# Kernel optimization log

Measured on AMD Instinct MI355X. Metric: run time of the kernel, lower is better.

The kernel has to match this reference:

```python
import jax, jax.numpy as jnp
import numpy as np


def setup_inputs() -> dict:
    key = jax.random.key(0)
    k1, k2, k3, k4, k5 = jax.random.split(key, 5)
    B, ENS, XDIM, YDIM = 8, 256, 8192, 256
    return {
        "Ens_ten": jax.random.normal(k1, (B, ENS, XDIM), dtype=jnp.float32),
        "H": jax.random.normal(k2, (XDIM, YDIM), dtype=jnp.float32),
        "y_true_mean": jax.random.normal(k3, (1, YDIM), dtype=jnp.float32),
        "y_true_std": jax.random.normal(k4, (1, YDIM), dtype=jnp.float32),
        "noise": jax.random.normal(k5, (B, YDIM, ENS), dtype=jnp.float32),
    }


def reference(Ens_ten, H, y_true_mean, y_true_std, noise):
    # Ens_ten: [b, ens, xdim]; H: [xdim, ydim]
    b, ens, xdim = Ens_ten.shape
    Y = jnp.einsum('bex,xy->bey', Ens_ten, H)          # observation_func (linear)
    x_m = jnp.mean(Ens_ten, axis=1, keepdims=True)     # [b,1,xdim]
    y_m = jnp.mean(Y, axis=1, keepdims=True)           # [b,1,ydim]
    Xc = jnp.swapaxes(Ens_ten - x_m, 1, 2)             # [b,xdim,ens]
    Yc = jnp.swapaxes(Y - y_m, 1, 2)                   # [b,ydim,ens]
    C_xy = jnp.einsum('bxe,bye->bxy', Xc, Yc) / ens    # [b,xdim,ydim]
    C_yy = jnp.einsum('bue,bve->buv', Yc, Yc) / ens    # [b,ydim,ydim]
    R = jnp.diag(jnp.square(y_true_std)[0])            # [ydim,ydim], broadcasts over batch
    A = R + C_yy                                       # [b,ydim,ydim]
    # torch.linalg.solve(A, C_xy, left=False): K = C_xy @ inv(A)
    K = jnp.swapaxes(
        jnp.linalg.solve(jnp.swapaxes(A, 1, 2), jnp.swapaxes(C_xy, 1, 2)), 1, 2
    )                                                  # [b,xdim,ydim]
    R_2 = noise * jnp.square(y_true_std)[:, :, None]   # [b,ydim,ens]
    innov = y_true_mean[:, :, None] - Yc + R_2         # [b,ydim,ens]
    update = jnp.einsum('bxy,bye->bxe', K, innov)      # [b,xdim,ens]
    return Ens_ten + jnp.swapaxes(update, 1, 2)
```

## Files before the change

### kernel.cpp

```cpp
#include <hip/hip_runtime.h>

#define ENSN 256
#define XDIM 8192
#define YD 256
#define BATCH 8

#define OFF_Y   0
#define OFF_YC  524288
#define OFF_AUG 1048576
#define OFF_W   2097152
#define OFF_XM  2621440

typedef __attribute__((ext_vector_type(4))) short short4v;
typedef __attribute__((ext_vector_type(8))) short short8v;
typedef __attribute__((ext_vector_type(4))) float float4v;

__device__ __forceinline__ unsigned short f2bf_rne(float x) {
    unsigned u = __float_as_uint(x);
    u += 0x7FFFu + ((u >> 16) & 1u);
    return (unsigned short)(u >> 16);
}

__global__ __launch_bounds__(256) void k1_colmean(const float* __restrict__ E,
                                                  float* __restrict__ xm) {
    int x = blockIdx.x * 256 + threadIdx.x;
    int b = blockIdx.y;
    const float* p = E + (size_t)b * ENSN * XDIM + x;
    float s = 0.f;
    #pragma unroll 8
    for (int e = 0; e < ENSN; e++) s += p[(size_t)e * XDIM];
    xm[b * XDIM + x] = s * (1.0f / ENSN);
}

__global__ __launch_bounds__(256) void kc_h(const float* __restrict__ H,
                                            short* __restrict__ Hthi,
                                            short* __restrict__ Htlo) {
    __shared__ float T[64][65];
    int k0 = blockIdx.x * 64, n0 = blockIdx.y * 64;
    int tid = threadIdx.x;
    int c = tid & 63, g = tid >> 6;
    #pragma unroll
    for (int p = 0; p < 16; p++)
        T[g + p * 4][c] = H[(size_t)(k0 + g + p * 4) * YD + n0 + c];
    __syncthreads();
    #pragma unroll
    for (int p = 0; p < 16; p++) {
        int nn = g + p * 4;
        float v = T[c][nn];
        unsigned short h = f2bf_rne(v);
        float hf = __uint_as_float(((unsigned)h) << 16);
        unsigned short l2 = f2bf_rne(v - hf);
        Hthi[(size_t)(n0 + nn) * XDIM + k0 + c] = (short)h;
        Htlo[(size_t)(n0 + nn) * XDIM + k0 + c] = (short)l2;
    }
}

#define EST 40
#define BST 40

__global__ __launch_bounds__(512, 2) void k2m_ygemm(const float* __restrict__ E,
                                                    const short* __restrict__ Hthi,
                                                    const short* __restrict__ Htlo,
                                                    float* __restrict__ Y) {
    __shared__ __align__(16) short Ehi[64 * EST];
    __shared__ __align__(16) short Elo[64 * EST];
    __shared__ __align__(16) short Bhi[256 * BST];
    __shared__ __align__(16) short Blo[256 * BST];
    int tid = threadIdx.x;
    int lane = tid & 63;
    int w = tid >> 6;
    int m0 = blockIdx.x * 64;
    int kb0 = blockIdx.y * 512;
    int wr = (w & 1) * 32;
    int wc = (w >> 1) * 64;
    float4v acc[8];
    #pragma unroll
    for (int i = 0; i < 8; i++) acc[i] = (float4v){0.f, 0.f, 0.f, 0.f};

    int erow = tid >> 3, ecol = (tid & 7) * 4;
    int brow = tid >> 1, bhalf = (tid & 1) * 16;
    int fr = lane & 15, fg = lane >> 4;

    for (int s = 0; s < 16; s++) {
        int kb = kb0 + s * 32;
        float4 ev = *(const float4*)&E[(size_t)(m0 + erow) * XDIM + kb + ecol];
        float vv[4] = {ev.x, ev.y, ev.z, ev.w};
        short4v hi4, lo4;
        #pragma unroll
        for (int j = 0; j < 4; j++) {
            unsigned short h = f2bf_rne(vv[j]);
            float hf = __uint_as_float(((unsigned)h) << 16);
            unsigned short l2 = f2bf_rne(vv[j] - hf);
            hi4[j] = (short)h; lo4[j] = (short)l2;
        }
        *(short4v*)&Ehi[erow * EST + ecol] = hi4;
        *(short4v*)&Elo[erow * EST + ecol] = lo4;
        short8v bh0 = *(const short8v*)&Hthi[(size_t)brow * XDIM + kb + bhalf];
        short8v bh1 = *(const short8v*)&Hthi[(size_t)brow * XDIM + kb + bhalf + 8];
        short8v bl0 = *(const short8v*)&Htlo[(size_t)brow * XDIM + kb + bhalf];
        short8v bl1 = *(const short8v*)&Htlo[(size_t)brow * XDIM + kb + bhalf + 8];
        *(short8v*)&Bhi[brow * BST + bhalf]     = bh0;
        *(short8v*)&Bhi[brow * BST + bhalf + 8] = bh1;
        *(short8v*)&Blo[brow * BST + bhalf]     = bl0;
        *(short8v*)&Blo[brow * BST + bhalf + 8] = bl1;
        __syncthreads();
        short8v ah[2], al[2], bhf[4], blf[4];
        #pragma unroll
        for (int ti = 0; ti < 2; ti++) {
            ah[ti] = *(const short8v*)&Ehi[(wr + ti * 16 + fr) * EST + fg * 8];
            al[ti] = *(const short8v*)&Elo[(wr + ti * 16 + fr) * EST + fg * 8];
        }
        #pragma unroll
        for (int tj = 0; tj < 4; tj++) {
            bhf[tj] = *(const short8v*)&Bhi[(wc + tj * 16 + fr) * BST + fg * 8];
            blf[tj] = *(const short8v*)&Blo[(wc + tj * 16 + fr) * BST + fg * 8];
        }
        #pragma unroll
        for (int ti = 0; ti < 2; ti++)
            #pragma unroll
            for (int tj = 0; tj < 4; tj++) {
                int a = ti * 4 + tj;
                acc[a] = __builtin_amdgcn_mfma_f32_16x16x32_bf16(ah[ti], bhf[tj], acc[a], 0, 0, 0);
                acc[a] = __builtin_amdgcn_mfma_f32_16x16x32_bf16(ah[ti], blf[tj], acc[a], 0, 0, 0);
                acc[a] = __builtin_amdgcn_mfma_f32_16x16x32_bf16(al[ti], bhf[tj], acc[a], 0, 0, 0);
            }
        __syncthreads();
    }
    #pragma unroll
    for (int ti = 0; ti < 2; ti++)
        #pragma unroll
        for (int tj = 0; tj < 4; tj++)
            #pragma unroll
            for (int q = 0; q < 4; q++) {
                int row = m0 + wr + ti * 16 + fg * 4 + q;
                int col = wc + tj * 16 + fr;
                atomicAdd(&Y[row * YD + col], acc[ti * 4 + tj][q]);
            }
}

__global__ __launch_bounds__(256) void k3_center(const float* __restrict__ Y,
                                                 const float* __restrict__ ytm,
                                                 const float* __restrict__ ystd,
                                                 const float* __restrict__ noise,
                                                 float* __restrict__ Yc,
                                                 float* __restrict__ aug) {
    int b = blockIdx.y, tid = threadIdx.x;
    int y0 = blockIdx.x * 64;
    __shared__ float red[4][64];
    __shared__ float ym[64], tms[64], s2[64];
    __shared__ float T[64][65];
    int yl = tid & 63, q = tid >> 6;
    float s = 0.f;
    for (int e = q * 64; e < q * 64 + 64; e++)
        s += Y[(size_t)(b * ENSN + e) * YD + y0 + yl];
    red[q][yl] = s;
    __syncthreads();
    if (tid < 64) {
        ym[tid] = (red[0][tid] + red[1][tid] + red[2][tid] + red[3][tid]) * (1.0f / ENSN);
        float sd = ystd[y0 + tid];
        s2[tid] = sd * sd;
        tms[tid] = ytm[y0 + tid];
    }
    __syncthreads();
    for (int e0 = 0; e0 < ENSN; e0 += 64) {
        #pragma unroll
        for (int p = 0; p < 16; p++) {
            int er = q + p * 4;
            T[er][yl] = Y[(size_t)(b * ENSN + e0 + er) * YD + y0 + yl];
        }
        __syncthreads();
        int ec = yl;
        #pragma unroll
        for (int p = 0; p < 16; p++) {
            int yr = q + p * 4;
            int y = y0 + yr, e = e0 + ec;
            float yv = T[ec][yr] - ym[yr];
            Yc[(size_t)b * YD * ENSN + (size_t)y * ENSN + e] = yv;
            aug[(size_t)b * YD * 512 + (size_t)y * 512 + 256 + e] =
                tms[yr] - yv + noise[(size_t)b * YD * ENSN + (size_t)y * ENSN + e] * s2[yr];
        }
        __syncthreads();
    }
}

__global__ __launch_bounds__(256) void k4_cyy(const float* __restrict__ Yc,
                                              const float* __restrict__ ystd,
                                              float* __restrict__ aug) {
    __shared__ float As[16][68];
    __shared__ float Bs[16][68];
    int tid = threadIdx.x;
    int m0 = blockIdx.x * 64, n0 = blockIdx.y * 64, b = blockIdx.z;
    const float* Ycb = Yc + (size_t)b * YD * ENSN;
    int tr = tid >> 4, tc = tid & 15;
    float acc[4][4];
    #pragma unroll
    for (int i = 0; i < 4; i++)
        #pragma unroll
        for (int j = 0; j < 4; j++) acc[i][j] = 0.f;
    int al = tid & 15, am0 = tid >> 4;
    for (int k0 = 0; k0 < ENSN; k0 += 16) {
        #pragma unroll
        for (int p = 0; p < 4; p++) {
            int am = am0 + p * 16;
            As[al][am] = Ycb[(m0 + am) * ENSN + k0 + al];
            Bs[al][am] = Ycb[(n0 + am) * ENSN + k0 + al];
        }
        __syncthreads();
        #pragma unroll
        for (int kk = 0; kk < 16; kk++) {
            float4 a = *(const float4*)&As[kk][tr * 4];
            float4 bb = *(const float4*)&Bs[kk][tc * 4];
            float af[4] = {a.x, a.y, a.z, a.w};
            float bf[4] = {bb.x, bb.y, bb.z, bb.w};
            #pragma unroll
            for (int i = 0; i < 4; i++)
                #pragma unroll
                for (int j = 0; j < 4; j++) acc[i][j] += af[i] * bf[j];
        }
        __syncthreads();
    }
    float* augb = aug + (size_t)b * YD * 512;
    #pragma unroll
    for (int i = 0; i < 4; i++) {
        int u = m0 + tr * 4 + i;
        #pragma unroll
        for (int j = 0; j < 4; j++) {
            int v = n0 + tc * 4 + j;
            float val = acc[i][j] * (1.0f / ENSN);
            if (u == v) { float sv = ystd[u]; val += sv * sv; }
            augb[u * 512 + v] = val;
        }
    }
}

#define RSTP 484
#define LSTP 233

__global__ __launch_bounds__(1024, 4) void k5p_panel(float* __restrict__ aug, int c0) {
    __shared__ __align__(16) float R[32 * RSTP];
    __shared__ float Ls[32 * LSTP];
    __shared__ __align__(16) float Dg[32 * 33];
    __shared__ float invd[32];
    int b = blockIdx.x, tid = threadIdx.x;
    float* A = aug + (size_t)b * 256 * 512;
    int r5 = tid >> 5, c5 = tid & 31;
    int WR = 480 - c0;
    int W2 = 224 - c0;

    Dg[r5 * 33 + c5] = A[(c0 + r5) * 512 + c0 + c5];
    __syncthreads();
    if (tid < 32) {
        float u[32];
        #pragma unroll
        for (int c = 0; c < 32; c++) u[c] = Dg[tid * 33 + c];
        for (int j = 0; j < 31; j++) {
            float pv = __shfl(u[j], j);
            float f = u[j] / pv;
            #pragma unroll
            for (int c = 0; c < 32; c++) {
                if (c > j) {
                    float ujc = __shfl(u[c], j);
                    if (tid > j) u[c] -= f * ujc;
                }
            }
            if (tid > j) u[j] = f;
        }
        #pragma unroll
        for (int c = 0; c < 32; c++) Dg[tid * 33 + c] = u[c];
        invd[tid] = 1.0f / u[tid];
    }
    for (int cc = c5; cc < WR; cc += 32)
        R[r5 * RSTP + cc] = A[(c0 + r5) * 512 + c0 + 32 + cc];
    for (int row = r5; row < W2; row += 32)
        Ls[c5 * LSTP + row] = A[(c0 + 32 + row) * 512 + c0 + c5];
    __syncthreads();
    A[(c0 + r5) * 512 + c0 + c5] = Dg[r5 * 33 + c5];
    if (tid < WR) {
        float y[32];
        #pragma unroll
        for (int j = 0; j < 32; j++) {
            float s = R[j * RSTP + tid];
            #pragma unroll
            for (int m = 0; m < 32; m++)
                if (m < j) s -= Dg[j * 33 + m] * y[m];
            y[j] = s;
        }
        #pragma unroll
        for (int j = 0; j < 32; j++)
            A[(c0 + j) * 512 + c0 + 32 + tid] = y[j];
    }
    if (tid >= 512 && tid < 512 + W2) {
        int row = tid - 512;
        float l[32];
        #pragma unroll
        for (int j = 0; j < 32; j++) {
            float s = Ls[j * LSTP + row];
            #pragma unroll
            for (int m = 0; m < 32; m++)
                if (m < j) s -= l[m] * Dg[m * 33 + j];
            l[j] = s * invd[j];
        }
        #pragma unroll
        for (int j = 0; j < 32; j++)
            Ls[j * LSTP + row] = l[j];
    }
    __syncthreads();
    for (int row = r5; row < W2; row += 32)
        A[(c0 + 32 + row) * 512 + c0 + c5] = Ls[c5 * LSTP + row];
}

__global__ __launch_bounds__(256) void k5t_trail(float* __restrict__ aug, int c0) {
    __shared__ __align__(16) float Lt[32][36];
    __shared__ __align__(16) float Ut[32][36];
    int b = blockIdx.z, tid = threadIdx.x;
    float* A = aug + (size_t)b * 256 * 512;
    int r0  = c0 + 32 + blockIdx.x * 32;
    int cc0 = c0 + 32 + blockIdx.y * 32;
    int lr = tid >> 3, lc = (tid & 7) * 4;
    *(float4*)&Lt[lr][lc] = *(const float4*)&A[(size_t)(r0 + lr) * 512 + c0 + lc];
    *(float4*)&Ut[lr][lc] = *(const float4*)&A[(size_t)(c0 + lr) * 512 + cc0 + lc];
    __syncthreads();
    float* gp = &A[(size_t)(r0 + lr) * 512 + cc0 + lc];
    float4 acc = *(const float4*)gp;
    #pragma unroll
    for (int k = 0; k < 32; k++) {
        float lv = Lt[lr][k];
        float4 uv = *(const float4*)&Ut[k][lc];
        acc.x -= lv * uv.x;
        acc.y -= lv * uv.y;
        acc.z -= lv * uv.z;
        acc.w -= lv * uv.w;
    }
    *(float4*)gp = acc;
}

#define ZST  68
#define LBST 36

__global__ __launch_bounds__(512, 2) void k5s_solve(float* __restrict__ aug) {
    __shared__ __align__(16) float Zs[256 * ZST];
    __shared__ __align__(16) float Lb[224 * LBST];
    __shared__ __align__(16) float Dg[32 * 33];
    __shared__ float invd[32];
    int b = blockIdx.y, tid = threadIdx.x;
    float* A = aug + (size_t)b * 256 * 512;
    int cb = blockIdx.x * 64;
    int c = tid & 63, g = tid >> 6;
    int rr = tid >> 5, cc = tid & 31;

    for (int r = g; r < 256; r += 8)
        Zs[r * ZST + c] = A[r * 512 + 256 + cb + c];

    for (int p = 7; p >= 0; p--) {
        int c0 = 32 * p, na = c0;
        for (int r = rr; r < 32; r += 16)
            Dg[r * 33 + cc] = A[(c0 + r) * 512 + c0 + cc];
        for (int r = rr; r < na; r += 16)
            Lb[r * LBST + cc] = A[r * 512 + c0 + cc];
        if (tid < 32)
            invd[tid] = 1.0f / A[(c0 + tid) * 512 + c0 + tid];
        __syncthreads();
        if (tid < 64) {
            float x[32];
            #pragma unroll
            for (int j = 31; j >= 0; j--) {
                float s = Zs[(c0 + j) * ZST + tid];
                #pragma unroll
                for (int m = 0; m < 32; m++)
                    if (m > j) s -= Dg[j * 33 + m] * x[m];
                x[j] = s * invd[j];
            }
            #pragma unroll
            for (int j = 0; j < 32; j++) Zs[(c0 + j) * ZST + tid] = x[j];
        }
        __syncthreads();
        if (na > 0) {
            float z[32];
            #pragma unroll
            for (int k = 0; k < 32; k++) z[k] = Zs[(c0 + k) * ZST + c];
            for (int r = g; r < na; r += 8) {
                const float* lp = &Lb[r * LBST];
                float a0 = 0.f, a1 = 0.f, a2 = 0.f, a3 = 0.f;
                #pragma unroll
                for (int k = 0; k < 32; k += 4) {
                    float4 lv = *(const float4*)(lp + k);
                    a0 += lv.x * z[k + 0];
                    a1 += lv.y * z[k + 1];
                    a2 += lv.z * z[k + 2];
                    a3 += lv.w * z[k + 3];
                }
                Zs[r * ZST + c] -= (a0 + a1) + (a2 + a3);
            }
        }
        __syncthreads();
    }

    for (int r = g; r < 256; r += 8)
        A[r * 512 + 256 + cb + c] = Zs[r * ZST + c];
}

__global__ __launch_bounds__(256) void k6_w(const float* __restrict__ Yc,
                                            const float* __restrict__ aug,
                                            float* __restrict__ W) {
    __shared__ float As[16][68];
    __shared__ float Bs[16][68];
    int tid = threadIdx.x;
    int m0 = blockIdx.x * 64, n0 = blockIdx.y * 64, b = blockIdx.z;
    const float* Ycb = Yc + (size_t)b * YD * ENSN;
    const float* augb = aug + (size_t)b * YD * 512;
    int tr = tid >> 4, tc = tid & 15;
    float acc[4][4];
    #pragma unroll
    for (int i = 0; i < 4; i++)
        #pragma unroll
        for (int j = 0; j < 4; j++) acc[i][j] = 0.f;
    int c = tid & 63, kr0 = tid >> 6;
    for (int k0 = 0; k0 < YD; k0 += 16) {
        #pragma unroll
        for (int p = 0; p < 4; p++) {
            int kk = kr0 + p * 4;
            As[kk][c] = Ycb[(k0 + kk) * ENSN + m0 + c];
            Bs[kk][c] = augb[(k0 + kk) * 512 + 256 + n0 + c];
        }
        __syncthreads();
        #pragma unroll
        for (int kk = 0; kk < 16; kk++) {
            float4 a = *(const float4*)&As[kk][tr * 4];
            float4 bb = *(const float4*)&Bs[kk][tc * 4];
            float af[4] = {a.x, a.y, a.z, a.w};
            float bf[4] = {bb.x, bb.y, bb.z, bb.w};
            #pragma unroll
            for (int i = 0; i < 4; i++)
                #pragma unroll
                for (int j = 0; j < 4; j++) acc[i][j] += af[i] * bf[j];
        }
        __syncthreads();
    }
    float* Wb = W + (size_t)b * ENSN * ENSN;
    #pragma unroll
    for (int i = 0; i < 4; i++)
        #pragma unroll
        for (int j = 0; j < 4; j++)
            Wb[(m0 + tr * 4 + i) * ENSN + n0 + tc * 4 + j] = acc[i][j] * (1.0f / ENSN);
}

__global__ __launch_bounds__(256, 4) void k7_update(const float* __restrict__ E,
                                                    const float* __restrict__ W,
                                                    const float* __restrict__ xm,
                                                    float* __restrict__ out) {
    __shared__ float As[16][260];
    __shared__ float Bs[16][68];
    __shared__ float xs[64];
    int tid = threadIdx.x;
    int x0 = blockIdx.x * 64;
    int b = blockIdx.y;
    const float* Wb = W + (size_t)b * ENSN * ENSN;
    const float* Eb = E + (size_t)b * ENSN * XDIM;
    if (tid < 64) xs[tid] = xm[b * XDIM + x0 + tid];
    __syncthreads();
    int tr = tid >> 4, tc = tid & 15;
    float acc[16][4];
    #pragma unroll
    for (int i = 0; i < 16; i++)
        #pragma unroll
        for (int j = 0; j < 4; j++) acc[i][j] = 0.f;
    for (int k0 = 0; k0 < ENSN; k0 += 16) {
        #pragma unroll
        for (int p = 0; p < 16; p++)
            As[p][tid] = Wb[(k0 + p) * ENSN + tid];
        #pragma unroll
        for (int p = 0; p < 4; p++) {
            int kk = (tid >> 6) + p * 4;
            int cc = tid & 63;
            Bs[kk][cc] = Eb[(size_t)(k0 + kk) * XDIM + x0 + cc] - xs[cc];
        }
        __syncthreads();
        #pragma unroll
        for (int kk = 0; kk < 16; kk++) {
            float4 bv = *(const float4*)&Bs[kk][tc * 4];
            float bf[4] = {bv.x, bv.y, bv.z, bv.w};
            #pragma unroll
            for (int q = 0; q < 4; q++) {
                float4 av = *(const float4*)&As[kk][tr * 16 + q * 4];
                float af[4] = {av.x, av.y, av.z, av.w};
                #pragma unroll
                for (int c2 = 0; c2 < 4; c2++)
                    #pragma unroll
                    for (int j = 0; j < 4; j++)
                        acc[q * 4 + c2][j] += af[c2] * bf[j];
            }
        }
        __syncthreads();
    }
    #pragma unroll
    for (int i = 0; i < 16; i++) {
        int e = tr * 16 + i;
        size_t idx = (size_t)(b * ENSN + e) * XDIM + x0 + tc * 4;
        float4 ev = *(const float4*)&E[idx];
        float4 ov;
        ov.x = ev.x + acc[i][0];
        ov.y = ev.y + acc[i][1];
        ov.z = ev.z + acc[i][2];
        ov.w = ev.w + acc[i][3];
        *(float4*)&out[idx] = ov;
    }
}

extern "C" void kernel_launch(void* const* d_in, const int* in_sizes, int n_in,
                              void* d_out, int out_size, void* d_ws, size_t ws_size,
                              hipStream_t stream) {
    const float* Ens   = (const float*)d_in[0];
    const float* H     = (const float*)d_in[1];
    const float* ytm   = (const float*)d_in[2];
    const float* ystd  = (const float*)d_in[3];
    const float* noise = (const float*)d_in[4];
    float* out = (float*)d_out;
    float* ws  = (float*)d_ws;

    float* Y   = ws + OFF_Y;
    float* Yc  = ws + OFF_YC;
    float* aug = ws + OFF_AUG;
    float* W   = ws + OFF_W;
    float* xm  = ws + OFF_XM;
    short* Hthi = (short*)(ws + 524288);
    short* Htlo = (short*)(ws + 1572864);

    hipMemsetAsync(Y, 0, (size_t)2048 * 256 * sizeof(float), stream);

    k1_colmean<<<dim3(XDIM / 256, BATCH), 256, 0, stream>>>(Ens, xm);
    kc_h<<<dim3(XDIM / 64, YD / 64), 256, 0, stream>>>(H, Hthi, Htlo);
    k2m_ygemm<<<dim3(2048 / 64, 16), 512, 0, stream>>>(Ens, Hthi, Htlo, Y);
    k3_center<<<dim3(4, BATCH), 256, 0, stream>>>(Y, ytm, ystd, noise, Yc, aug);
    k4_cyy<<<dim3(4, 4, BATCH), 256, 0, stream>>>(Yc, ystd, aug);
    for (int p = 0; p < 8; p++) {
        k5p_panel<<<dim3(BATCH), 1024, 0, stream>>>(aug, 32 * p);
        if (p < 7)
            k5t_trail<<<dim3(7 - p, 15 - p, BATCH), 256, 0, stream>>>(aug, 32 * p);
    }
    k5s_solve<<<dim3(4, BATCH), 512, 0, stream>>>(aug);
    k6_w<<<dim3(4, 4, BATCH), 256, 0, stream>>>(Yc, aug, W);
    k7_update<<<dim3(XDIM / 64, BATCH), 256, 0, stream>>>(Ens, W, xm, out);
}
```

Baseline: 743.1 us.

## Run final ensemble update GEMM on bf16x3 MFMA with pre-split transposed W

Replaces the FP32 FMA update kernel with an MFMA-based kernel that splits both W and the centered ensemble into bf16 hi/lo parts and accumulates three bf16 products, which approximates FP32 accuracy. A new small kernel transposes W and splits it into hi/lo bf16 buffers, reusing the Y workspace region. The aim is to move the large update GEMM (8x256x256x8192) onto the matrix cores. The costs are an extra launch, the extra hi/lo conversion work, and a scalar, less coalesced output store pattern.

```diff
diff --git a/kernel.cpp b/kernel.cpp
--- a/kernel.cpp
+++ b/kernel.cpp
@@ -444,66 +444,116 @@
             Wb[(m0 + tr * 4 + i) * ENSN + n0 + tc * 4 + j] = acc[i][j] * (1.0f / ENSN);
 }
 
-__global__ __launch_bounds__(256, 4) void k7_update(const float* __restrict__ E,
-                                                    const float* __restrict__ W,
-                                                    const float* __restrict__ xm,
-                                                    float* __restrict__ out) {
-    __shared__ float As[16][260];
-    __shared__ float Bs[16][68];
+__global__ __launch_bounds__(256) void kw_w(const float* __restrict__ W,
+                                            short* __restrict__ Wthi,
+                                            short* __restrict__ Wtlo) {
+    __shared__ float T[64][65];
+    int f0 = blockIdx.x * 64, e0 = blockIdx.y * 64, b = blockIdx.z;
+    const float* Wb = W + (size_t)b * ENSN * ENSN;
+    int tid = threadIdx.x;
+    int c = tid & 63, g = tid >> 6;
+    #pragma unroll
+    for (int p = 0; p < 16; p++)
+        T[g + p * 4][c] = Wb[(size_t)(f0 + g + p * 4) * ENSN + e0 + c];
+    __syncthreads();
+    #pragma unroll
+    for (int p = 0; p < 16; p++) {
+        int ee = g + p * 4;
+        float v = T[c][ee];
+        unsigned short h = f2bf_rne(v);
+        float hf = __uint_as_float(((unsigned)h) << 16);
+        unsigned short l2 = f2bf_rne(v - hf);
+        size_t o = (size_t)b * ENSN * ENSN + (size_t)(e0 + ee) * ENSN + f0 + c;
+        Wthi[o] = (short)h;
+        Wtlo[o] = (short)l2;
+    }
+}
+
+#define WST 36
+#define XST 36
+
+__global__ __launch_bounds__(512, 2) void k7m_update(const float* __restrict__ E,
+                                                     const short* __restrict__ Wthi,
+                                                     const short* __restrict__ Wtlo,
+                                                     const float* __restrict__ xm,
+                                                     float* __restrict__ out) {
+    __shared__ __align__(16) short Ahi[256 * WST];
+    __shared__ __align__(16) short Alo[256 * WST];
+    __shared__ __align__(16) short Bhi[64 * XST];
+    __shared__ __align__(16) short Blo[64 * XST];
     __shared__ float xs[64];
     int tid = threadIdx.x;
+    int lane = tid & 63;
+    int w = tid >> 6;
     int x0 = blockIdx.x * 64;
     int b = blockIdx.y;
-    const float* Wb = W + (size_t)b * ENSN * ENSN;
+    const short* Whb = Wthi + (size_t)b * ENSN * ENSN;
+    const short* Wlb = Wtlo + (size_t)b * ENSN * ENSN;
     const float* Eb = E + (size_t)b * ENSN * XDIM;
     if (tid < 64) xs[tid] = xm[b * XDIM + x0 + tid];
     __syncthreads();
-    int tr = tid >> 4, tc = tid & 15;
-    float acc[16][4];
-    #pragma unroll
-    for (int i = 0; i < 16; i++)
-        #pragma unroll
-        for (int j = 0; j < 4; j++) acc[i][j] = 0.f;
-    for (int k0 = 0; k0 < ENSN; k0 += 16) {
-        #pragma unroll
-        for (int p = 0; p < 16; p++)
-            As[p][tid] = Wb[(k0 + p) * ENSN + tid];
-        #pragma unroll
-        for (int p = 0; p < 4; p++) {
-            int kk = (tid >> 6) + p * 4;
-            int cc = tid & 63;
-            Bs[kk][cc] = Eb[(size_t)(k0 + kk) * XDIM + x0 + cc] - xs[cc];
-        }
-        __syncthreads();
-        #pragma unroll
-        for (int kk = 0; kk < 16; kk++) {
-            float4 bv = *(const float4*)&Bs[kk][tc * 4];
-            float bf[4] = {bv.x, bv.y, bv.z, bv.w};
+    int wr = (w & 3) * 64;
+    int wc = (w >> 2) * 32;
+    float4v acc[8];
+    #pragma unroll
+    for (int i = 0; i < 8; i++) acc[i] = (float4v){0.f, 0.f, 0.f, 0.f};
+    int fr = lane & 15, fg = lane >> 4;
+    int ae = tid >> 2, ach = (tid & 3) * 8;
+    int bx = tid & 63, bkq = tid >> 6;
+
+    for (int s = 0; s < 8; s++) {
+        int k0 = s * 32;
+        #pragma unroll
+        for (int h = 0; h < 2; h++) {
+            int e = ae + h * 128;
+            *(short8v*)&Ahi[e * WST + ach] = *(const short8v*)&Whb[(size_t)e * ENSN + k0 + ach];
+            *(short8v*)&Alo[e * WST + ach] = *(const short8v*)&Wlb[(size_t)e * ENSN + k0 + ach];
+        }
+        short4v hi4, lo4;
+        #pragma unroll
+        for (int j = 0; j < 4; j++) {
+            float v = Eb[(size_t)(k0 + bkq * 4 + j) * XDIM + x0 + bx] - xs[bx];
+            unsigned short h = f2bf_rne(v);
+            float hf = __uint_as_float(((unsigned)h) << 16);
+            unsigned short l2 = f2bf_rne(v - hf);
+            hi4[j] = (short)h; lo4[j] = (short)l2;
+        }
+        *(short4v*)&Bhi[bx * XST + bkq * 4] = hi4;
+        *(short4v*)&Blo[bx * XST + bkq * 4] = lo4;
+        __syncthreads();
+        short8v ah[4], al[4], bhf[2], blf[2];
+        #pragma unroll
+        for (int ti = 0; ti < 4; ti++) {
+            ah[ti] = *(const short8v*)&Ahi[(wr + ti * 16 + fr) * WST + fg * 8];
+            al[ti] = *(const short8v*)&Alo[(wr + ti * 16 + fr) * WST + fg * 8];
+        }
+        #pragma unroll
+        for (int tj = 0; tj < 2; tj++) {
+            bhf[tj] = *(const short8v*)&Bhi[(wc + tj * 16 + fr) * XST + fg * 8];
+            blf[tj] = *(const short8v*)&Blo[(wc + tj * 16 + fr) * XST + fg * 8];
+        }
+        #pragma unroll
+        for (int ti = 0; ti < 4; ti++)
+            #pragma unroll
+            for (int tj = 0; tj < 2; tj++) {
+                int a = ti * 2 + tj;
+                acc[a] = __builtin_amdgcn_mfma_f32_16x16x32_bf16(ah[ti], bhf[tj], acc[a], 0, 0, 0);
+                acc[a] = __builtin_amdgcn_mfma_f32_16x16x32_bf16(ah[ti], blf[tj], acc[a], 0, 0, 0);
+                acc[a] = __builtin_amdgcn_mfma_f32_16x16x32_bf16(al[ti], bhf[tj], acc[a], 0, 0, 0);
+            }
+        __syncthreads();
+    }
+    #pragma unroll
+    for (int ti = 0; ti < 4; ti++)
+        #pragma unroll
+        for (int tj = 0; tj < 2; tj++)
             #pragma unroll
             for (int q = 0; q < 4; q++) {
-                float4 av = *(const float4*)&As[kk][tr * 16 + q * 4];
-                float af[4] = {av.x, av.y, av.z, av.w};
-                #pragma unroll
-                for (int c2 = 0; c2 < 4; c2++)
-                    #pragma unroll
-                    for (int j = 0; j < 4; j++)
-                        acc[q * 4 + c2][j] += af[c2] * bf[j];
-            }
-        }
-        __syncthreads();
-    }
-    #pragma unroll
-    for (int i = 0; i < 16; i++) {
-        int e = tr * 16 + i;
-        size_t idx = (size_t)(b * ENSN + e) * XDIM + x0 + tc * 4;
-        float4 ev = *(const float4*)&E[idx];
-        float4 ov;
-        ov.x = ev.x + acc[i][0];
-        ov.y = ev.y + acc[i][1];
-        ov.z = ev.z + acc[i][2];
-        ov.w = ev.w + acc[i][3];
-        *(float4*)&out[idx] = ov;
-    }
+                int e = wr + ti * 16 + fg * 4 + q;
+                int x = x0 + wc + tj * 16 + fr;
+                size_t idx = (size_t)(b * ENSN + e) * XDIM + x;
+                out[idx] = E[idx] + acc[ti * 2 + tj][q];
+            }
 }
 
 extern "C" void kernel_launch(void* const* d_in, const int* in_sizes, int n_in,
@@ -524,6 +574,8 @@
     float* xm  = ws + OFF_XM;
     short* Hthi = (short*)(ws + 524288);
     short* Htlo = (short*)(ws + 1572864);
+    short* Wthi = (short*)(ws + 0);
+    short* Wtlo = (short*)(ws + 262144);
 
     hipMemsetAsync(Y, 0, (size_t)2048 * 256 * sizeof(float), stream);
 
@@ -539,5 +591,6 @@
     }
     k5s_solve<<<dim3(4, BATCH), 512, 0, stream>>>(aug);
     k6_w<<<dim3(4, 4, BATCH), 256, 0, stream>>>(Yc, aug, W);
-    k7_update<<<dim3(XDIM / 64, BATCH), 256, 0, stream>>>(Ens, W, xm, out);
-}
+    kw_w<<<dim3(4, 4, BATCH), 256, 0, stream>>>(W, Wthi, Wtlo);
+    k7m_update<<<dim3(XDIM / 64, BATCH), 512, 0, stream>>>(Ens, Wthi, Wtlo, xm, out);
+}
```

After: 697.5 us. 6.1% less time.
